# Performance work log

Hardware: AMD Instinct MI355X
Metric: run time of the kernel (lower is better)

The kernel has to match this reference:

```python
import jax, jax.numpy as jnp
import numpy as np
from jax import lax

DIM = 192
HEADS = 8
HID = int(DIM * 4.0)

def setup_inputs() -> dict:
    key = jax.random.key(0)
    ks = jax.random.split(key, 10)
    b, c, h, w = 4, DIM, 256, DIM  # w must equal dim for the Mlp over last axis
    x = jax.random.normal(ks[0], (b, c, h, w), dtype=jnp.float32)
    return {
        "x": x,
        "ln1_w": jnp.ones((DIM,), jnp.float32),
        "ln1_b": jnp.zeros((DIM,), jnp.float32),
        "temperature": jnp.ones((HEADS, 1, 1), jnp.float32),
        "qkv_w": jax.random.normal(ks[1], (3 * DIM, DIM), jnp.float32) * 0.02,
        "dw_w": jax.random.normal(ks[2], (3 * DIM, 1, 3, 3), jnp.float32) * 0.1,
        "proj_w": jax.random.normal(ks[3], (DIM, DIM), jnp.float32) * 0.02,
        "ln2_w": jnp.ones((DIM,), jnp.float32),
        "ln2_b": jnp.zeros((DIM,), jnp.float32),
        "fc1_w": jax.random.normal(ks[4], (HID, DIM), jnp.float32) * 0.02,
        "fc1_b": jnp.zeros((HID,), jnp.float32),
        "fc2_w": jax.random.normal(ks[5], (DIM, HID), jnp.float32) * 0.02,
        "fc2_b": jnp.zeros((DIM,), jnp.float32),
    }

def _layernorm_chan(x, w, b):
    # WithBias LayerNorm over the channel axis, per spatial location (to_3d -> LN -> to_4d)
    mu = jnp.mean(x, axis=1, keepdims=True)
    var = jnp.mean((x - mu) ** 2, axis=1, keepdims=True)
    y = (x - mu) / jnp.sqrt(var + 1e-5)
    return y * w[None, :, None, None] + b[None, :, None, None]

def _l2norm(x, axis=-1, eps=1e-12):
    n = jnp.sqrt(jnp.sum(x * x, axis=axis, keepdims=True))
    return x / jnp.maximum(n, eps)

def _attention(x, temperature, qkv_w, dw_w, proj_w):
    b, c, h, w = x.shape
    # 1x1 conv (pointwise GEMM) then 3x3 depthwise conv
    qkv = jnp.einsum('oc,bchw->bohw', qkv_w, x)
    qkv = lax.conv_general_dilated(qkv, dw_w, window_strides=(1, 1), padding='SAME',
                                   feature_group_count=3 * c,
                                   dimension_numbers=('NCHW', 'OIHW', 'NCHW'))
    q, k, v = jnp.split(qkv, 3, axis=1)
    ch = c // HEADS
    q = q.reshape(b, HEADS, ch, h * w)
    k = k.reshape(b, HEADS, ch, h * w)
    v = v.reshape(b, HEADS, ch, h * w)
    q = _l2norm(q)
    k = _l2norm(k)
    attn = jnp.einsum('bhcn,bhdn->bhcd', q, k) * temperature  # [b,H,ch,ch] channel attention
    attn = jax.nn.softmax(attn, axis=-1)
    out = jnp.einsum('bhcd,bhdn->bhcn', attn, v).reshape(b, c, h, w)
    return jnp.einsum('oc,bchw->bohw', proj_w, out)

def _mlp(x, fc1_w, fc1_b, fc2_w, fc2_b):
    # nn.Linear applied on the LAST axis (w == dim), matching the original quirk
    h1 = jnp.einsum('bchw,ow->bcho', x, fc1_w) + fc1_b
    h1 = jax.nn.gelu(h1, approximate=False)
    return jnp.einsum('bcho,do->bchd', h1, fc2_w) + fc2_b

def reference(x, ln1_w, ln1_b, temperature, qkv_w, dw_w, proj_w, ln2_w, ln2_b, fc1_w, fc1_b, fc2_w, fc2_b):
    x = x + _attention(_layernorm_chan(x, ln1_w, ln1_b), temperature, qkv_w, dw_w, proj_w)
    x = x + _mlp(_layernorm_chan(x, ln2_w, ln2_b), fc1_w, fc1_b, fc2_w, fc2_b)
    return x
```

## Files before the change

kernel.cpp:

```cpp
#include <hip/hip_runtime.h>
#include <math.h>

#define SSP   49152
#define HDIM  256
#define WDIM  192
#define CDIM  192
#define NHEAD 8
#define CH    24
#define OC3   576
#define HIDF  768
#define NB    4
#define SCCH  24

typedef short bf16x8 __attribute__((ext_vector_type(8)));
typedef float f32x4  __attribute__((ext_vector_type(4)));

__device__ inline short f2bf(float f) {
  unsigned u = __float_as_uint(f);
  u += 0x7fffu + ((u >> 16) & 1u);
  return (short)(u >> 16);
}
__device__ inline float bf2f(short h) {
  return __uint_as_float(((unsigned)(unsigned short)h) << 16);
}

__global__ __launch_bounds__(256) void cvt_bf16(const float* __restrict__ in,
                                                short* __restrict__ out, int n) {
  int i = blockIdx.x * 256 + threadIdx.x;
  if (i < n) out[i] = f2bf(in[i]);
}

__global__ __launch_bounds__(256) void ln_to_bf16T(const float* __restrict__ x,
                                                   const float* __restrict__ w,
                                                   const float* __restrict__ b,
                                                   short* __restrict__ yt) {
  int s = blockIdx.x * 256 + threadIdx.x;
  int bz = blockIdx.y;
  const float* xb = x + (size_t)bz * CDIM * SSP;
  float sum = 0.f, sq = 0.f;
  for (int c = 0; c < CDIM; ++c) {
    float v = xb[(size_t)c * SSP + s];
    sum += v; sq += v * v;
  }
  float mu = sum * (1.f / CDIM);
  float rstd = rsqrtf(sq * (1.f / CDIM) - mu * mu + 1e-5f);
  short* yp = yt + (size_t)bz * SSP * CDIM + (size_t)s * CDIM;
  for (int c8 = 0; c8 < CDIM / 8; ++c8) {
    bf16x8 v;
#pragma unroll
    for (int j = 0; j < 8; ++j) {
      int c = c8 * 8 + j;
      v[j] = f2bf((xb[(size_t)c * SSP + s] - mu) * rstd * w[c] + b[c]);
    }
    *(bf16x8*)(yp + c8 * 8) = v;
  }
}

__global__ __launch_bounds__(256) void ln_to_bf16N(const float* __restrict__ x,
                                                   const float* __restrict__ w,
                                                   const float* __restrict__ b,
                                                   short* __restrict__ y) {
  int s = blockIdx.x * 256 + threadIdx.x;
  int bz = blockIdx.y;
  const float* xb = x + (size_t)bz * CDIM * SSP;
  short* yb = y + (size_t)bz * CDIM * SSP;
  float sum = 0.f, sq = 0.f;
  for (int c = 0; c < CDIM; ++c) {
    float v = xb[(size_t)c * SSP + s];
    sum += v; sq += v * v;
  }
  float mu = sum * (1.f / CDIM);
  float rstd = rsqrtf(sq * (1.f / CDIM) - mu * mu + 1e-5f);
  for (int c = 0; c < CDIM; ++c) {
    float v = xb[(size_t)c * SSP + s];
    yb[(size_t)c * SSP + s] = f2bf((v - mu) * rstd * w[c] + b[c]);
  }
}

template <int BM, int BN, int WM, int WN, bool RESID, bool OUT_BF16>
__global__ __launch_bounds__(256) void mfma_gemm(
    const short* __restrict__ A, const short* __restrict__ B,
    const float* __restrict__ resid, void* __restrict__ Cv,
    int M, int N, int K, long long strideB, long long strideC) {
  constexpr int BK = 32, PAD = 40;
  constexpr int WTM = BM / WM, WTN = BN / WN;
  constexpr int FM = WTM / 16, FN = WTN / 16;
  static_assert(WM * WN == 4 && BM % 64 == 0 && BN % 64 == 0, "cfg");
  __shared__ short As[BM * PAD];
  __shared__ short Bs[BN * PAD];
  const int tid = threadIdx.x;
  const int m0 = blockIdx.y * BM, n0 = blockIdx.x * BN;
  const long long z = blockIdx.z;
  const short* Bz = B + z * strideB;
  const int w = tid >> 6, lane = tid & 63;
  const int wm = w / WN, wn = w % WN;
  const int r16 = lane & 15, kg = lane >> 4;
  const int arow = tid >> 2, akc = tid & 3;

  f32x4 acc[FM][FN] = {};

  for (int k0 = 0; k0 < K; k0 += BK) {
#pragma unroll
    for (int i = 0; i < BM; i += 64) {
      bf16x8 v = *(const bf16x8*)(A + (size_t)(m0 + i + arow) * K + k0 + akc * 8);
      *(bf16x8*)(&As[(i + arow) * PAD + akc * 8]) = v;
    }
#pragma unroll
    for (int i = 0; i < BN; i += 64) {
      bf16x8 v = *(const bf16x8*)(Bz + (size_t)(n0 + i + arow) * K + k0 + akc * 8);
      *(bf16x8*)(&Bs[(i + arow) * PAD + akc * 8]) = v;
    }
    __syncthreads();
    bf16x8 af[FM], bfr[FN];
#pragma unroll
    for (int i = 0; i < FM; ++i)
      af[i] = *(bf16x8*)(&As[(wm * WTM + i * 16 + r16) * PAD + kg * 8]);
#pragma unroll
    for (int j = 0; j < FN; ++j)
      bfr[j] = *(bf16x8*)(&Bs[(wn * WTN + j * 16 + r16) * PAD + kg * 8]);
#pragma unroll
    for (int i = 0; i < FM; ++i)
#pragma unroll
      for (int j = 0; j < FN; ++j)
        acc[i][j] = __builtin_amdgcn_mfma_f32_16x16x32_bf16(af[i], bfr[j], acc[i][j], 0, 0, 0);
    __syncthreads();
  }

  float* Cf = (float*)Cv + z * strideC;
  short* Ch = (short*)Cv + z * strideC;
  const float* R = RESID ? resid + z * strideC : nullptr;
#pragma unroll
  for (int i = 0; i < FM; ++i) {
#pragma unroll
    for (int j = 0; j < FN; ++j) {
#pragma unroll
      for (int t = 0; t < 4; ++t) {
        int m = m0 + wm * WTM + i * 16 + kg * 4 + t;
        int n = n0 + wn * WTN + j * 16 + r16;
        float v = acc[i][j][t];
        size_t idx = (size_t)m * N + n;
        if (RESID) v += R[idx];
        if (OUT_BF16) Ch[idx] = f2bf(v); else Cf[idx] = v;
      }
    }
  }
}

__global__ __launch_bounds__(256) void dwconv_tile(const short* __restrict__ in,
                                                   const float* __restrict__ w9,
                                                   short* __restrict__ out) {
  __shared__ short tile[34][208];
  const int tid = threadIdx.x;
  const int ch = blockIdx.x >> 3;
  const int slab = blockIdx.x & 7;
  const int o = ch % OC3;
  const int y0 = slab * 32;
  float wr[9];
#pragma unroll
  for (int i = 0; i < 9; ++i) wr[i] = w9[o * 9 + i];
  const short* ip = in + (size_t)ch * SSP;

  if (tid < 34) { tile[tid][7] = 0; tile[tid][200] = 0; }
#pragma unroll
  for (int i = 0; i < 4; ++i) {
    int idx = i * 256 + tid;
    if (idx < 816) {
      int row = idx / 24, cx = idx - row * 24;
      int gy = y0 + row - 1;
      bf16x8 v = {};
      if (gy >= 0 && gy < HDIM) v = *(const bf16x8*)(ip + gy * WDIM + cx * 8);
      *(bf16x8*)(&tile[row][8 + cx * 8]) = v;
    }
  }
  __syncthreads();

  short* op = out + (size_t)ch * SSP;
#pragma unroll
  for (int g = 0; g < 3; ++g) {
    int G = g * 256 + tid;
    int r = G / 24, cx = G - (G / 24) * 24;
    int cb = cx * 8 + 7;
    float a[10], b[10], c[10];
#pragma unroll
    for (int d = 0; d < 10; ++d) {
      a[d] = bf2f(tile[r][cb + d]);
      b[d] = bf2f(tile[r + 1][cb + d]);
      c[d] = bf2f(tile[r + 2][cb + d]);
    }
    bf16x8 ov;
#pragma unroll
    for (int j = 0; j < 8; ++j) {
      float acc = wr[0] * a[j] + wr[1] * a[j + 1] + wr[2] * a[j + 2]
                + wr[3] * b[j] + wr[4] * b[j + 1] + wr[5] * b[j + 2]
                + wr[6] * c[j] + wr[7] * c[j + 1] + wr[8] * c[j + 2];
      ov[j] = f2bf(acc);
    }
    *(bf16x8*)(op + (y0 + r) * WDIM + cx * 8) = ov;
  }
}

__global__ __launch_bounds__(256) void scores_stage1(const short* __restrict__ D,
                                                     float* __restrict__ pdot,
                                                     float* __restrict__ qss,
                                                     float* __restrict__ kss) {
  int ch = blockIdx.x, h = blockIdx.y, b = blockIdx.z;
  __shared__ float qs[24][260];
  __shared__ float ks[24][260];
  int tid = threadIdx.x;
  int w = tid >> 6, lane = tid & 63;
  int c0 = w * 6;
  float acc[6] = {0.f, 0.f, 0.f, 0.f, 0.f, 0.f};
  float ssacc = 0.f;
  const short* qb = D + ((size_t)b * OC3 + h * CH) * SSP;
  const short* kb = D + ((size_t)b * OC3 + CDIM + h * CH) * SSP;
  for (int it = 0; it < 8; ++it) {
    int s0 = ch * 2048 + it * 256;
#pragma unroll
    for (int p = 0; p < 3; ++p) {
      int u = p * 256 + tid;
      int row = u >> 5, col8 = u & 31;
      bf16x8 qv = *(const bf16x8*)(qb + (size_t)row * SSP + s0 + col8 * 8);
      bf16x8 kv = *(const bf16x8*)(kb + (size_t)row * SSP + s0 + col8 * 8);
#pragma unroll
      for (int j = 0; j < 8; ++j) {
        qs[row][col8 * 8 + j] = bf2f(qv[j]);
        ks[row][col8 * 8 + j] = bf2f(kv[j]);
      }
    }
    __syncthreads();
    if (w < 2 && lane < 24) {
      const float (*src)[260] = (w == 0) ? qs : ks;
      for (int s = 0; s < 256; s += 4) {
        float4 v = *(const float4*)&src[lane][s];
        ssacc += v.x * v.x + v.y * v.y + v.z * v.z + v.w * v.w;
      }
    }
    if (lane < 24) {
      for (int s = 0; s < 256; s += 4) {
        float4 kv = *(float4*)&ks[lane][s];
#pragma unroll
        for (int i = 0; i < 6; ++i) {
          float4 qv = *(float4*)&qs[c0 + i][s];
          acc[i] += qv.x * kv.x + qv.y * kv.y + qv.z * kv.z + qv.w * kv.w;
        }
      }
    }
    __syncthreads();
  }
  if (lane < 24) {
    float* pb = pdot + (size_t)b * (NHEAD * CH * CH * SCCH);
#pragma unroll
    for (int i = 0; i < 6; ++i)
      pb[(((size_t)h * CH + (c0 + i)) * CH + lane) * SCCH + ch] = acc[i];
    if (w == 0) qss[(((size_t)b * NHEAD + h) * CH + lane) * SCCH + ch] = ssacc;
    if (w == 1) kss[(((size_t)b * NHEAD + h) * CH + lane) * SCCH + ch] = ssacc;
  }
}

__global__ void scores_reduce(const float* __restrict__ pdot,
                              const float* __restrict__ qss,
                              const float* __restrict__ kss,
                              const float* __restrict__ temp,
                              float* __restrict__ atn) {
  int c = blockIdx.x, h = blockIdx.y, b = blockIdx.z;
  int tid = threadIdx.x;
  __shared__ float row[24];
  if (tid < 24) {
    const float* p = pdot + (size_t)b * (NHEAD * CH * CH * SCCH) +
                     (((size_t)h * CH + c) * CH + tid) * SCCH;
    float s = 0.f;
#pragma unroll
    for (int i = 0; i < SCCH; ++i) s += p[i];
    const float* pq = qss + (((size_t)b * NHEAD + h) * CH + c) * SCCH;
    const float* pk = kss + (((size_t)b * NHEAD + h) * CH + tid) * SCCH;
    float sq = 0.f, sk = 0.f;
#pragma unroll
    for (int i = 0; i < SCCH; ++i) { sq += pq[i]; sk += pk[i]; }
    float rq = 1.f / fmaxf(sqrtf(sq), 1e-12f);
    float rk = 1.f / fmaxf(sqrtf(sk), 1e-12f);
    row[tid] = s * rq * rk * temp[h];
  }
  __syncthreads();
  if (tid < 24) {
    float mx = -1e30f;
    for (int d = 0; d < 24; ++d) mx = fmaxf(mx, row[d]);
    float sum = 0.f;
    for (int d = 0; d < 24; ++d) sum += expf(row[d] - mx);
    atn[((size_t)b * NHEAD + h) * 576 + c * CH + tid] = expf(row[tid] - mx) / sum;
  }
}

__global__ __launch_bounds__(256) void attn_pv_bf16(const short* __restrict__ D,
                                                    const float* __restrict__ atn,
                                                    short* __restrict__ pvt) {
  int nb = blockIdx.x, h = blockIdx.y, b = blockIdx.z;
  __shared__ float aL[24][24];
  int tid = threadIdx.x;
  const float* ab = atn + ((size_t)b * NHEAD + h) * 576;
  for (int i = tid; i < 576; i += 256) aL[i / 24][i % 24] = ab[i];
  __syncthreads();
  int n = nb * 256 + tid;
  const short* vb = D + ((size_t)b * OC3 + 2 * CDIM + h * CH) * SSP + n;
  float vv[24];
#pragma unroll
  for (int d = 0; d < 24; ++d) vv[d] = bf2f(vb[(size_t)d * SSP]);
  short* ob = pvt + (size_t)b * SSP * CDIM + (size_t)n * CDIM + h * CH;
  bf16x8 o0, o1, o2;
#pragma unroll
  for (int cc = 0; cc < 24; ++cc) {
    float s = 0.f;
#pragma unroll
    for (int d = 0; d < 24; ++d) s += aL[cc][d] * vv[d];
    short bv = f2bf(s);
    if (cc < 8) o0[cc & 7] = bv; else if (cc < 16) o1[cc & 7] = bv; else o2[cc & 7] = bv;
  }
  *(bf16x8*)(ob) = o0;
  *(bf16x8*)(ob + 8) = o1;
  *(bf16x8*)(ob + 16) = o2;
}

__global__ __launch_bounds__(512) void mlp_fused(const short* __restrict__ y2,
                                                 const short* __restrict__ w1,
                                                 const short* __restrict__ w2,
                                                 const float* __restrict__ b1,
                                                 const float* __restrict__ b2,
                                                 float* __restrict__ out) {
  __shared__ short y2s[128 * 200];
  __shared__ short w1s[64 * 200];
  __shared__ short w2s[192 * 72];
  __shared__ short h1s[128 * 72];
  const int tid = threadIdx.x;
  const int m0 = blockIdx.x * 128;
  const int w = tid >> 6, lane = tid & 63;
  const int r16 = lane & 15, kg = lane >> 4;
  const int wm = w >> 1;
  const int wn = w & 1;

#pragma unroll
  for (int it = 0; it < 6; ++it) {
    int u = it * 512 + tid;
    int row = u / 24, cx = u % 24;
    bf16x8 v = *(const bf16x8*)(y2 + (size_t)(m0 + row) * CDIM + cx * 8);
    *(bf16x8*)(&y2s[row * 200 + cx * 8]) = v;
  }

  f32x4 bacc[2][6] = {};

  for (int hc = 0; hc < 12; ++hc) {
#pragma unroll
    for (int it = 0; it < 3; ++it) {
      int u = it * 512 + tid;
      int row = u / 24, cx = u % 24;
      bf16x8 v = *(const bf16x8*)(w1 + (size_t)(hc * 64 + row) * CDIM + cx * 8);
      *(bf16x8*)(&w1s[row * 200 + cx * 8]) = v;
      int row2 = u / 8, cx2 = u % 8;
      bf16x8 v2 = *(const bf16x8*)(w2 + (size_t)row2 * HIDF + hc * 64 + cx2 * 8);
      *(bf16x8*)(&w2s[row2 * 72 + cx2 * 8]) = v2;
    }
    __syncthreads();

    f32x4 pacc[2][2] = {};
#pragma unroll
    for (int ks = 0; ks < 6; ++ks) {
      bf16x8 af[2], bg[2];
#pragma unroll
      for (int i = 0; i < 2; ++i)
        af[i] = *(bf16x8*)(&y2s[(wm * 32 + i * 16 + r16) * 200 + ks * 32 + kg * 8]);
#pragma unroll
      for (int j = 0; j < 2; ++j)
        bg[j] = *(bf16x8*)(&w1s[(wn * 32 + j * 16 + r16) * 200 + ks * 32 + kg * 8]);
#pragma unroll
      for (int i = 0; i < 2; ++i)
#pragma unroll
        for (int j = 0; j < 2; ++j)
          pacc[i][j] = __builtin_amdgcn_mfma_f32_16x16x32_bf16(af[i], bg[j], pacc[i][j], 0, 0, 0);
    }
#pragma unroll
    for (int i = 0; i < 2; ++i)
#pragma unroll
      for (int j = 0; j < 2; ++j)
#pragma unroll
        for (int t = 0; t < 4; ++t) {
          int mr = wm * 32 + i * 16 + kg * 4 + t;
          int nc = wn * 32 + j * 16 + r16;
          float v = pacc[i][j][t] + b1[hc * 64 + nc];
          v = 0.5f * v * (1.f + erff(v * 0.70710678118654752f));
          h1s[mr * 72 + nc] = f2bf(v);
        }
    __syncthreads();

#pragma unroll
    for (int ks = 0; ks < 2; ++ks) {
      bf16x8 a2[2];
#pragma unroll
      for (int i = 0; i < 2; ++i)
        a2[i] = *(bf16x8*)(&h1s[(wm * 32 + i * 16 + r16) * 72 + ks * 32 + kg * 8]);
#pragma unroll
      for (int j = 0; j < 6; ++j) {
        bf16x8 b2g = *(bf16x8*)(&w2s[(wn * 96 + j * 16 + r16) * 72 + ks * 32 + kg * 8]);
#pragma unroll
        for (int i = 0; i < 2; ++i)
          bacc[i][j] = __builtin_amdgcn_mfma_f32_16x16x32_bf16(a2[i], b2g, bacc[i][j], 0, 0, 0);
      }
    }
    __syncthreads();
  }

#pragma unroll
  for (int i = 0; i < 2; ++i)
#pragma unroll
    for (int j = 0; j < 6; ++j)
#pragma unroll
      for (int t = 0; t < 4; ++t) {
        int m = m0 + wm * 32 + i * 16 + kg * 4 + t;
        int n = wn * 96 + j * 16 + r16;
        size_t idx = (size_t)m * CDIM + n;
        out[idx] = bacc[i][j][t] + b2[n] + out[idx];
      }
}

extern "C" void kernel_launch(void* const* d_in, const int* in_sizes, int n_in,
                              void* d_out, int out_size, void* d_ws, size_t ws_size,
                              hipStream_t stream) {
  const float* x      = (const float*)d_in[0];
  const float* ln1_w  = (const float*)d_in[1];
  const float* ln1_b  = (const float*)d_in[2];
  const float* temp   = (const float*)d_in[3];
  const float* qkv_w  = (const float*)d_in[4];
  const float* dw_w   = (const float*)d_in[5];
  const float* proj_w = (const float*)d_in[6];
  const float* ln2_w  = (const float*)d_in[7];
  const float* ln2_b  = (const float*)d_in[8];
  const float* fc1_w  = (const float*)d_in[9];
  const float* fc1_b  = (const float*)d_in[10];
  const float* fc2_w  = (const float*)d_in[11];
  const float* fc2_b  = (const float*)d_in[12];
  float* out = (float*)d_out;

  char* base = (char*)d_ws;
  short* wq  = (short*)base;
  short* wp  = wq + 110592;
  short* w1  = wp + 36864;
  short* w2  = w1 + 147456;
  float* pdot= (float*)(base + 890880);
  float* qss = (float*)(base + 2660352);
  float* kss = (float*)(base + 2734080);
  float* atn = (float*)(base + 2807808);
  short* Dv  = (short*)(base + 4194304);
  short* y1t = Dv;
  short* T   = (short*)(base + 230686720);
  short* pvt = T;
  short* y2  = (short*)(base + 457179136);

  cvt_bf16<<<dim3(432), 256, 0, stream>>>(qkv_w, wq, 110592);
  cvt_bf16<<<dim3(144), 256, 0, stream>>>(proj_w, wp, 36864);
  cvt_bf16<<<dim3(576), 256, 0, stream>>>(fc1_w, w1, 147456);
  cvt_bf16<<<dim3(576), 256, 0, stream>>>(fc2_w, w2, 147456);

  ln_to_bf16T<<<dim3(SSP / 256, NB), 256, 0, stream>>>(x, ln1_w, ln1_b, y1t);
  mfma_gemm<64, 256, 1, 4, false, true><<<dim3(SSP / 256, OC3 / 64, NB), 256, 0, stream>>>(
      wq, y1t, nullptr, T, OC3, SSP, CDIM, (long long)SSP * CDIM, (long long)OC3 * SSP);
  dwconv_tile<<<dim3(NB * OC3 * 8), 256, 0, stream>>>(T, dw_w, Dv);
  scores_stage1<<<dim3(SCCH, NHEAD, NB), 256, 0, stream>>>(Dv, pdot, qss, kss);
  scores_reduce<<<dim3(CH, NHEAD, NB), 64, 0, stream>>>(pdot, qss, kss, temp, atn);
  attn_pv_bf16<<<dim3(SSP / 256, NHEAD, NB), 256, 0, stream>>>(Dv, atn, pvt);
  mfma_gemm<64, 256, 1, 4, true, false><<<dim3(SSP / 256, CDIM / 64, NB), 256, 0, stream>>>(
      wp, pvt, x, out, CDIM, SSP, CDIM, (long long)SSP * CDIM, (long long)CDIM * SSP);
  ln_to_bf16N<<<dim3(SSP / 256, NB), 256, 0, stream>>>(out, ln2_w, ln2_b, y2);
  mlp_fused<<<dim3(196608 / 128), 512, 0, stream>>>(y2, w1, w2, fc1_b, fc2_b, out);
}
```

Baseline: 1.017 ms.

## Prefetch next MLP weight chunk into registers and vectorize hidden-activation stores

The fused MLP kernel now loads the next hidden chunk's fc1/fc2 weight tiles from global memory into registers while the current chunk computes, then writes them to shared memory after the second GEMM. This is meant to hide global-load latency behind MFMA work. The first GEMM's MFMA operands are swapped so each lane holds four consecutive hidden columns, which lets the GELU outputs go to shared memory as packed 4-element stores instead of scalar ones. The cost is more registers per thread, which may lower occupancy, plus an extra barrier per iteration.

```diff
diff --git a/kernel.cpp b/kernel.cpp
--- a/kernel.cpp
+++ b/kernel.cpp
@@ -13,6 +13,7 @@
 #define SCCH  24
 
 typedef short bf16x8 __attribute__((ext_vector_type(8)));
+typedef short bf16x4 __attribute__((ext_vector_type(4)));
 typedef float f32x4  __attribute__((ext_vector_type(4)));
 
 __device__ inline short f2bf(float f) {
@@ -336,6 +337,12 @@
   const int wm = w >> 1;
   const int wn = w & 1;
 
+  const int u0 = tid, u1 = 512 + tid, u2 = 1024 + tid;
+  const int s1r[3] = {u0 / 24, u1 / 24, u2 / 24};
+  const int s1c[3] = {u0 % 24, u1 % 24, u2 % 24};
+  const int s2r[3] = {u0 / 8, u1 / 8, u2 / 8};
+  const int s2c[3] = {u0 % 8, u1 % 8, u2 % 8};
+
 #pragma unroll
   for (int it = 0; it < 6; ++it) {
     int u = it * 512 + tid;
@@ -343,21 +350,26 @@
     bf16x8 v = *(const bf16x8*)(y2 + (size_t)(m0 + row) * CDIM + cx * 8);
     *(bf16x8*)(&y2s[row * 200 + cx * 8]) = v;
   }
+#pragma unroll
+  for (int it = 0; it < 3; ++it) {
+    bf16x8 v = *(const bf16x8*)(w1 + (size_t)s1r[it] * CDIM + s1c[it] * 8);
+    *(bf16x8*)(&w1s[s1r[it] * 200 + s1c[it] * 8]) = v;
+    bf16x8 v2 = *(const bf16x8*)(w2 + (size_t)s2r[it] * HIDF + s2c[it] * 8);
+    *(bf16x8*)(&w2s[s2r[it] * 72 + s2c[it] * 8]) = v2;
+  }
+  __syncthreads();
 
   f32x4 bacc[2][6] = {};
+  bf16x8 rw1[3], rw2[3];
 
   for (int hc = 0; hc < 12; ++hc) {
-#pragma unroll
-    for (int it = 0; it < 3; ++it) {
-      int u = it * 512 + tid;
-      int row = u / 24, cx = u % 24;
-      bf16x8 v = *(const bf16x8*)(w1 + (size_t)(hc * 64 + row) * CDIM + cx * 8);
-      *(bf16x8*)(&w1s[row * 200 + cx * 8]) = v;
-      int row2 = u / 8, cx2 = u % 8;
-      bf16x8 v2 = *(const bf16x8*)(w2 + (size_t)row2 * HIDF + hc * 64 + cx2 * 8);
-      *(bf16x8*)(&w2s[row2 * 72 + cx2 * 8]) = v2;
-    }
-    __syncthreads();
+    if (hc < 11) {
+#pragma unroll
+      for (int it = 0; it < 3; ++it) {
+        rw1[it] = *(const bf16x8*)(w1 + (size_t)((hc + 1) * 64 + s1r[it]) * CDIM + s1c[it] * 8);
+        rw2[it] = *(const bf16x8*)(w2 + (size_t)s2r[it] * HIDF + (hc + 1) * 64 + s2c[it] * 8);
+      }
+    }
 
     f32x4 pacc[2][2] = {};
 #pragma unroll
@@ -373,20 +385,24 @@
       for (int i = 0; i < 2; ++i)
 #pragma unroll
         for (int j = 0; j < 2; ++j)
-          pacc[i][j] = __builtin_amdgcn_mfma_f32_16x16x32_bf16(af[i], bg[j], pacc[i][j], 0, 0, 0);
-    }
-#pragma unroll
-    for (int i = 0; i < 2; ++i)
-#pragma unroll
-      for (int j = 0; j < 2; ++j)
+          pacc[i][j] = __builtin_amdgcn_mfma_f32_16x16x32_bf16(bg[j], af[i], pacc[i][j], 0, 0, 0);
+    }
+#pragma unroll
+    for (int i = 0; i < 2; ++i) {
+      int mr = wm * 32 + i * 16 + r16;
+#pragma unroll
+      for (int j = 0; j < 2; ++j) {
+        int hid0 = wn * 32 + j * 16 + kg * 4;
+        bf16x4 pk;
 #pragma unroll
         for (int t = 0; t < 4; ++t) {
-          int mr = wm * 32 + i * 16 + kg * 4 + t;
-          int nc = wn * 32 + j * 16 + r16;
-          float v = pacc[i][j][t] + b1[hc * 64 + nc];
+          float v = pacc[i][j][t] + b1[hc * 64 + hid0 + t];
           v = 0.5f * v * (1.f + erff(v * 0.70710678118654752f));
-          h1s[mr * 72 + nc] = f2bf(v);
+          pk[t] = f2bf(v);
         }
+        *(bf16x4*)(&h1s[mr * 72 + hid0]) = pk;
+      }
+    }
     __syncthreads();
 
 #pragma unroll
@@ -404,6 +420,15 @@
       }
     }
     __syncthreads();
+
+    if (hc < 11) {
+#pragma unroll
+      for (int it = 0; it < 3; ++it) {
+        *(bf16x8*)(&w1s[s1r[it] * 200 + s1c[it] * 8]) = rw1[it];
+        *(bf16x8*)(&w2s[s2r[it] * 72 + s2c[it] * 8]) = rw2[it];
+      }
+      __syncthreads();
+    }
   }
 
 #pragma unroll
```

New measurement: 1.015 ms. About the same (-0.2%).
